# Kernel optimization log

Hardware: AMD Instinct MI355X
Metric: run time of the kernel (lower is better)

The kernel has to match this reference:

```python
import jax, jax.numpy as jnp
import numpy as np

K_DIM = 1024
HEADS = 16


def setup_inputs() -> dict:
    key = jax.random.key(0)
    kx, kw1, kb1, kw2, kb2 = jax.random.split(key, 5)
    b, t, k = 4, 2048, K_DIM
    scale = 1.0 / np.sqrt(k)
    x = jax.random.normal(kx, (b, t, k), dtype=jnp.float32)
    # torch nn.Linear params: weight [out, in], bias [out]
    W_qkv = jax.random.normal(kw1, (3 * k, k), dtype=jnp.float32) * scale
    b_qkv = jax.random.normal(kb1, (3 * k,), dtype=jnp.float32) * scale
    W_out = jax.random.normal(kw2, (k, k), dtype=jnp.float32) * scale
    b_out = jax.random.normal(kb2, (k,), dtype=jnp.float32) * scale
    return {"x": x, "W_qkv": W_qkv, "b_qkv": b_qkv, "W_out": W_out, "b_out": b_out}


def reference(x, W_qkv, b_qkv, W_out, b_out):
    b, t, k = x.shape
    h = HEADS
    s = k // h
    # tokqv linear: [b,t,3k]
    kqv = jnp.einsum('btk,ok->bto', x, W_qkv) + b_qkv
    # view [b,t,h,3s] -> transpose -> [b,h,t,3s], then split q,k,v along last dim
    kqv = kqv.reshape(b, t, h, 3 * s).transpose(0, 2, 1, 3)
    q, kk, v = kqv[..., :s], kqv[..., s:2 * s], kqv[..., 2 * s:]
    scores = jnp.einsum('bhqd,bhkd->bhqk', q, kk) / jnp.sqrt(jnp.float32(s * h))  # note: scale uses full k per source (queries.size(-1)=s, but here head dim s)
    # Faithful: original attention scales by sqrt(queries.size(-1)) = sqrt(s)
    scores = jnp.einsum('bhqd,bhkd->bhqk', q, kk) / jnp.sqrt(jnp.float32(s))
    weights = jax.nn.softmax(scores, axis=-1)
    res = jnp.einsum('bhqk,bhkd->bhqd', weights, v)  # [b,h,t,s]
    res = res.transpose(0, 2, 1, 3).reshape(b, t, k)
    return jnp.einsum('btk,ok->bto', res, W_out) + b_out
```

## Files before the change

### kernel.cpp

```cpp
#include <hip/hip_runtime.h>
#include <hip/hip_bf16.h>

typedef float  f32x4  __attribute__((ext_vector_type(4)));
typedef float  f32x8  __attribute__((ext_vector_type(8)));
typedef float  f32x16 __attribute__((ext_vector_type(16)));
typedef __bf16 bf16x8 __attribute__((ext_vector_type(8)));
typedef unsigned short u16x4 __attribute__((ext_vector_type(4)));
typedef unsigned short u16x8 __attribute__((ext_vector_type(8)));
typedef unsigned int   u32x4 __attribute__((ext_vector_type(4)));

#define QSCALE 0.18033688011112042f

__device__ __forceinline__ unsigned short f2bf(float f) {
  __bf16 h = (__bf16)f;
  return __builtin_bit_cast(unsigned short, h);
}

__device__ __forceinline__ f32x4 mfma16(bf16x8 a, bf16x8 b, f32x4 c) {
  return __builtin_amdgcn_mfma_f32_16x16x32_bf16(a, b, c, 0, 0, 0);
}
__device__ __forceinline__ f32x16 mfma32(bf16x8 a, bf16x8 b, f32x16 c) {
  return __builtin_amdgcn_mfma_f32_32x32x16_bf16(a, b, c, 0, 0, 0);
}
__device__ __forceinline__ f32x16 zero16() {
  f32x16 v;
#pragma unroll
  for (int i = 0; i < 16; ++i) v[i] = 0.f;
  return v;
}

typedef const __attribute__((address_space(1))) void* gptr_t;
typedef __attribute__((address_space(3))) void* lptr_t;
__device__ __forceinline__ void gld16(const void* g, void* l) {
  __builtin_amdgcn_global_load_lds((gptr_t)g, (lptr_t)l, 16, 0, 0);
}


__global__ __launch_bounds__(256) void prep_x(const float* __restrict__ x,
                                              unsigned short* __restrict__ A1) {
  const int mb = blockIdx.x >> 5;
  const int kB = blockIdx.x & 31;
#pragma unroll
  for (int ph = 0; ph < 2; ++ph) {
    int c = threadIdx.x + ph * 256;
    int lg = c >> 7, r = c & 127;
    f32x8 v = *(const f32x8*)(x + (size_t)(mb * 128 + r) * 1024 + kB * 32 + lg * 8);
    u16x8 h;
#pragma unroll
    for (int j = 0; j < 8; ++j) h[j] = f2bf(v[j]);
    *(u16x8*)(A1 + (size_t)(mb * 32 + kB) * 4096 + (size_t)c * 8) = h;
  }
}

__global__ __launch_bounds__(256) void prep_w(const float* __restrict__ w,
                                              unsigned short* __restrict__ o) {
  const int rb = blockIdx.x >> 5;
  const int kB = blockIdx.x & 31;
#pragma unroll
  for (int ph = 0; ph < 2; ++ph) {
    int c = threadIdx.x + ph * 256;
    int lg = c >> 7, r = c & 127;
    f32x8 v = *(const f32x8*)(w + (size_t)(rb * 128 + r) * 1024 + kB * 32 + lg * 8);
    u16x8 h;
#pragma unroll
    for (int j = 0; j < 8; ++j) h[j] = f2bf(v[j]);
    *(u16x8*)(o + (size_t)(rb * 32 + kB) * 4096 + (size_t)c * 8) = h;
  }
}

template <int EPI, int MINW>
__global__ __launch_bounds__(256, MINW) void gemm_bt(
    const __bf16* __restrict__ A, const __bf16* __restrict__ B,
    const float* __restrict__ bias, int N, int nbx, int NT,
    unsigned short* __restrict__ q_out, unsigned short* __restrict__ k_out,
    unsigned short* __restrict__ v_out, float* __restrict__ f_out) {
  __shared__ __align__(16) char smem[3 * 16384];
  const int tid = threadIdx.x;
  const int lane = tid & 63;
  const int wave = tid >> 6;
  const int ln = lane & 15, lg = lane >> 4;
  const int wm = wave >> 1;
  const int wn = wave & 1;
  const int bm = blockIdx.x / nbx;
  const int bn = blockIdx.x % nbx;

  f32x4 acc[4][4];
#pragma unroll
  for (int i = 0; i < 4; ++i)
#pragma unroll
    for (int j = 0; j < 4; ++j) acc[i][j] = (f32x4){0.f, 0.f, 0.f, 0.f};

  const __bf16* Asrc = A + ((size_t)bm * NT) * 4096 + tid * 8;
  const __bf16* Bsrc = B + ((size_t)bn * NT) * 4096 + tid * 8;
  const int aoff = lg * 2048 + (wm * 64 + ln) * 16;
  const int boff = 8192 + lg * 2048 + (wn * 64 + ln) * 16;

#define STAGE(slot_, tf_)                                                      \
  do {                                                                         \
    char* d_ = smem + (slot_) * 16384;                                         \
    const __bf16* a_ = Asrc + (size_t)(tf_) * 4096;                            \
    const __bf16* b_ = Bsrc + (size_t)(tf_) * 4096;                            \
    gld16(a_, d_ + tid * 16);                                                  \
    gld16(a_ + 2048, d_ + 4096 + tid * 16);                                    \
    gld16(b_, d_ + 8192 + tid * 16);                                           \
    gld16(b_ + 2048, d_ + 12288 + tid * 16);                                   \
  } while (0)

#define KBODY(t_, scur_, snxt_)                                                \
  do {                                                                         \
    int tf_ = ((t_) + 2 < NT) ? (t_) + 2 : NT - 1;                             \
    STAGE(snxt_, tf_);                                                         \
    const char* ab_ = smem + (scur_) * 16384;                                  \
    bf16x8 af_[4], bq_[4];                                                     \
    _Pragma("unroll") for (int mi = 0; mi < 4; ++mi)                           \
        af_[mi] = *(const bf16x8*)(ab_ + aoff + mi * 256);                     \
    _Pragma("unroll") for (int ni = 0; ni < 4; ++ni)                           \
        bq_[ni] = *(const bf16x8*)(ab_ + boff + ni * 256);                     \
    __builtin_amdgcn_s_setprio(1);                                             \
    _Pragma("unroll") for (int mi = 0; mi < 4; ++mi)                           \
        _Pragma("unroll") for (int ni = 0; ni < 4; ++ni)                       \
            acc[mi][ni] = mfma16(af_[mi], bq_[ni], acc[mi][ni]);               \
    __builtin_amdgcn_s_setprio(0);                                             \
    asm volatile("s_waitcnt vmcnt(4)\n\ts_barrier" ::: "memory");              \
  } while (0)

  STAGE(0, 0);
  STAGE(1, 1);
  asm volatile("s_waitcnt vmcnt(4)\n\ts_barrier" ::: "memory");

  for (int t = 0; t < NT; t += 3) {
    KBODY(t, 0, 2);
    if (t + 1 < NT) KBODY(t + 1, 1, 0);
    if (t + 2 < NT) KBODY(t + 2, 2, 1);
  }
  asm volatile("s_waitcnt vmcnt(0)" ::: "memory");
#undef KBODY
#undef STAGE

#pragma unroll
  for (int mi = 0; mi < 4; ++mi) {
#pragma unroll
    for (int ni = 0; ni < 4; ++ni) {
      int n = bn * 128 + wn * 64 + ni * 16 + ln;
      float bv = bias[n];
#pragma unroll
      for (int j = 0; j < 4; ++j) {
        int m = bm * 128 + wm * 64 + mi * 16 + lg * 4 + j;
        float val = acc[mi][ni][j] + bv;
        if constexpr (EPI == 0) {
          int h = n / 192;
          int r3 = n - h * 192;
          int b = m >> 11;
          int t = m & 2047;
          size_t base = (size_t)(b * 16 + h) << 17;
          if (r3 < 64) {
            q_out[base + ((size_t)t << 6) + r3] = f2bf(val * QSCALE);
          } else if (r3 < 128) {
            int d = r3 - 64;
            size_t off = base + (size_t)(t >> 6) * 4096 +
                         (size_t)((((t >> 5) & 1) << 2) + (d >> 4)) * 512 +
                         ((d >> 3) & 1) * 256 + (t & 31) * 8 + (d & 7);
            k_out[off] = f2bf(val);
          } else {
            int c = r3 - 128;
            size_t off = base + (size_t)(t >> 6) * 4096 +
                         (size_t)(((c >> 5) << 2) + ((t >> 4) & 3)) * 512 +
                         ((t >> 3) & 1) * 256 + (c & 31) * 8 + (t & 7);
            v_out[off] = f2bf(val);
          }
        } else {
          f_out[(size_t)m * N + n] = val;
        }
      }
    }
  }
}

__global__ __launch_bounds__(512, 4) void attn2(
    const __bf16* __restrict__ Q, const __bf16* __restrict__ Kg,
    const __bf16* __restrict__ Vg, unsigned short* __restrict__ res) {
  __shared__ __align__(16) char smem[3 * 16384];
  const int tid = threadIdx.x;
  const int lane = tid & 63;
  const int wq = tid >> 6;
  const int l31 = lane & 31;
  const int hi = lane >> 5;
  const int bh = blockIdx.x & 63;
  const int q0 = (blockIdx.x >> 6) << 8;
  const size_t bh_elem = (size_t)bh << 17;

  const __bf16* Kbh = Kg + bh_elem;
  const __bf16* Vbh = Vg + bh_elem;

  bf16x8 qf[4];
  {
    const __bf16* qrow = Q + bh_elem + ((size_t)(q0 + wq * 32 + l31) << 6) + hi * 8;
#pragma unroll
    for (int ks = 0; ks < 4; ++ks) qf[ks] = *(const bf16x8*)(qrow + ks * 16);
  }
  const u16x8 one8 = {0x3F80, 0x3F80, 0x3F80, 0x3F80,
                      0x3F80, 0x3F80, 0x3F80, 0x3F80};
  const bf16x8 ones = __builtin_bit_cast(bf16x8, one8);

  const f32x16 fz = zero16();
  f32x16 oacc0 = zero16(), oacc1 = zero16(), lacc = zero16();

#define AST(slot_, t_)                                                         \
  do {                                                                         \
    char* sb_ = smem + (slot_) * 16384;                                        \
    gld16(Kbh + (size_t)(t_) * 4096 + tid * 8, sb_ + tid * 16);                \
    gld16(Vbh + (size_t)(t_) * 4096 + tid * 8, sb_ + 8192 + tid * 16);         \
  } while (0)

  AST(0, 0);
  AST(1, 1);
  asm volatile("s_waitcnt vmcnt(2)\n\ts_barrier" ::: "memory");

  const int t2rev = wq & 1;
  int sc = 0;
  for (int tile = 0; tile < 32; ++tile) {
    int tf = (tile + 2 < 32) ? tile + 2 : 31;
    int sn = sc + 2; if (sn >= 3) sn -= 3;
    AST(sn, tf);

    const char* kbase = smem + sc * 16384;
    const char* vbase = kbase + 8192;
    const int loff = hi * 512 + l31 * 16;

#pragma unroll
    for (int tt = 0; tt < 2; ++tt) {
      const int t2 = tt ^ t2rev;
      f32x16 s;
      __builtin_amdgcn_s_setprio(1);
      {
        bf16x8 kf0 = *(const bf16x8*)(kbase + (t2 * 4) * 1024 + loff);
        s = mfma32(kf0, qf[0], fz);
      }
#pragma unroll
      for (int ks = 1; ks < 4; ++ks) {
        bf16x8 kf = *(const bf16x8*)(kbase + (t2 * 4 + ks) * 1024 + loff);
        s = mfma32(kf, qf[ks], s);
      }
      __builtin_amdgcn_s_setprio(0);
      float p[16];
#pragma unroll
      for (int r = 0; r < 16; ++r) p[r] = __builtin_amdgcn_exp2f(s[r]);
      unsigned int pk[8];
#pragma unroll
      for (int i = 0; i < 8; ++i)
        pk[i] = ((unsigned int)f2bf(p[2 * i + 1]) << 16) | f2bf(p[2 * i]);
      asm volatile("v_permlane32_swap_b32 %0, %1" : "+v"(pk[0]), "+v"(pk[2]));
      asm volatile("v_permlane32_swap_b32 %0, %1" : "+v"(pk[1]), "+v"(pk[3]));
      asm volatile("v_permlane32_swap_b32 %0, %1" : "+v"(pk[4]), "+v"(pk[6]));
      asm volatile("v_permlane32_swap_b32 %0, %1" : "+v"(pk[5]), "+v"(pk[7]));
      __builtin_amdgcn_s_setprio(1);
#pragma unroll
      for (int ks2 = 0; ks2 < 2; ++ks2) {
        u32x4 bw = {pk[ks2 * 4 + 0], pk[ks2 * 4 + 1],
                    pk[ks2 * 4 + 2], pk[ks2 * 4 + 3]};
        bf16x8 pb = __builtin_bit_cast(bf16x8, bw);
        int kb2 = t2 * 2 + ks2;
        bf16x8 v0 = *(const bf16x8*)(vbase + (kb2) * 1024 + loff);
        bf16x8 v1 = *(const bf16x8*)(vbase + (4 + kb2) * 1024 + loff);
        lacc  = mfma32(ones, pb, lacc);
        oacc0 = mfma32(v0, pb, oacc0);
        oacc1 = mfma32(v1, pb, oacc1);
      }
      __builtin_amdgcn_s_setprio(0);
    }
    asm volatile("s_waitcnt vmcnt(2)\n\ts_barrier" ::: "memory");
    sc = (sc + 1 == 3) ? 0 : sc + 1;
  }
  asm volatile("s_waitcnt vmcnt(0)" ::: "memory");
#undef AST

  float rl = __builtin_amdgcn_rcpf(lacc[0]);
  const int b = bh >> 4, h = bh & 15;
  const int rloc = wq * 32 + l31;
  const int mb = b * 16 + (blockIdx.x >> 6) * 2 + (rloc >> 7);
  const int r = rloc & 127;
  unsigned short* c0 = res + (size_t)(mb * 32 + 2 * h) * 4096 + r * 8 + hi * 4;
#pragma unroll
  for (int g = 0; g < 4; ++g) {
    u16x4 st0, st1;
#pragma unroll
    for (int rr = 0; rr < 4; ++rr) {
      st0[rr] = f2bf(oacc0[g * 4 + rr] * rl);
      st1[rr] = f2bf(oacc1[g * 4 + rr] * rl);
    }
    *(u16x4*)(c0 + g * 1024) = st0;
    *(u16x4*)(c0 + 4096 + g * 1024) = st1;
  }
}

extern "C" void kernel_launch(void* const* d_in, const int* in_sizes, int n_in,
                              void* d_out, int out_size, void* d_ws, size_t ws_size,
                              hipStream_t stream) {
  const float* x    = (const float*)d_in[0];
  const float* Wqkv = (const float*)d_in[1];
  const float* bqkv = (const float*)d_in[2];
  const float* Wout = (const float*)d_in[3];
  const float* bout = (const float*)d_in[4];
  float* out = (float*)d_out;
  char* ws = (char*)d_ws;

  unsigned short* A1 = (unsigned short*)(ws);
  unsigned short* B1 = (unsigned short*)(ws + 50331648);
  unsigned short* Qb = (unsigned short*)(ws + 69206016);
  unsigned short* Kb = (unsigned short*)(ws + 85983232);
  unsigned short* Vb = (unsigned short*)(ws + 102760448);
  unsigned short* Rb = (unsigned short*)(ws + 119537664);
  unsigned short* Wo = (unsigned short*)(ws + 136314880);

  prep_x<<<64 * 32, 256, 0, stream>>>(x, A1);
  prep_w<<<24 * 32, 256, 0, stream>>>(Wqkv, B1);
  prep_w<<<8 * 32, 256, 0, stream>>>(Wout, Wo);

  gemm_bt<0, 3><<<64 * 24, 256, 0, stream>>>((const __bf16*)A1, (const __bf16*)B1,
                                             bqkv, 3072, 24, 32,
                                             Qb, Kb, Vb, nullptr);

  attn2<<<512, 512, 0, stream>>>((const __bf16*)Qb, (const __bf16*)Kb,
                                 (const __bf16*)Vb, Rb);

  gemm_bt<1, 2><<<64 * 8, 256, 0, stream>>>((const __bf16*)Rb, (const __bf16*)Wo,
                                            bout, 1024, 8, 32,
                                            nullptr, nullptr, nullptr, out);
}
```

Before: 186.4 us.

## Process two 32-row query blocks per wave in attention kernel

Halves the attention block to 256 threads and has each wave handle 64 query rows (two 32-row Q fragments), so every K and V fragment read from LDS feeds two MFMAs. This is meant to cut LDS read traffic per unit of compute and raise the MFMA-to-load ratio. The cost is more live accumulators and registers per wave, fewer waves per block and lower occupancy (launch bounds 256,2), and twice as many async loads per thread, with the vmcnt waits adjusted to match.

```diff
diff --git a/kernel.cpp b/kernel.cpp
--- a/kernel.cpp
+++ b/kernel.cpp
@@ -176,7 +176,7 @@
   }
 }
 
-__global__ __launch_bounds__(512, 4) void attn2(
+__global__ __launch_bounds__(256, 2) void attn2(
     const __bf16* __restrict__ Q, const __bf16* __restrict__ Kg,
     const __bf16* __restrict__ Vg, unsigned short* __restrict__ res) {
   __shared__ __align__(16) char smem[3 * 16384];
@@ -192,29 +192,37 @@
   const __bf16* Kbh = Kg + bh_elem;
   const __bf16* Vbh = Vg + bh_elem;
 
-  bf16x8 qf[4];
+  bf16x8 qf0[4], qf1[4];
   {
-    const __bf16* qrow = Q + bh_elem + ((size_t)(q0 + wq * 32 + l31) << 6) + hi * 8;
-#pragma unroll
-    for (int ks = 0; ks < 4; ++ks) qf[ks] = *(const bf16x8*)(qrow + ks * 16);
+    const __bf16* qr0 = Q + bh_elem + ((size_t)(q0 + wq * 64 + l31) << 6) + hi * 8;
+    const __bf16* qr1 = qr0 + (32 << 6);
+#pragma unroll
+    for (int ks = 0; ks < 4; ++ks) {
+      qf0[ks] = *(const bf16x8*)(qr0 + ks * 16);
+      qf1[ks] = *(const bf16x8*)(qr1 + ks * 16);
+    }
   }
   const u16x8 one8 = {0x3F80, 0x3F80, 0x3F80, 0x3F80,
                       0x3F80, 0x3F80, 0x3F80, 0x3F80};
   const bf16x8 ones = __builtin_bit_cast(bf16x8, one8);
 
   const f32x16 fz = zero16();
-  f32x16 oacc0 = zero16(), oacc1 = zero16(), lacc = zero16();
+  f32x16 oA0 = zero16(), oA1 = zero16(), lA = zero16();
+  f32x16 oB0 = zero16(), oB1 = zero16(), lB = zero16();
 
 #define AST(slot_, t_)                                                         \
   do {                                                                         \
     char* sb_ = smem + (slot_) * 16384;                                        \
-    gld16(Kbh + (size_t)(t_) * 4096 + tid * 8, sb_ + tid * 16);                \
-    gld16(Vbh + (size_t)(t_) * 4096 + tid * 8, sb_ + 8192 + tid * 16);         \
+    _Pragma("unroll") for (int it_ = 0; it_ < 2; ++it_) {                      \
+      int idx_ = tid + it_ * 256;                                              \
+      gld16(Kbh + (size_t)(t_) * 4096 + idx_ * 8, sb_ + idx_ * 16);            \
+      gld16(Vbh + (size_t)(t_) * 4096 + idx_ * 8, sb_ + 8192 + idx_ * 16);     \
+    }                                                                          \
   } while (0)
 
   AST(0, 0);
   AST(1, 1);
-  asm volatile("s_waitcnt vmcnt(2)\n\ts_barrier" ::: "memory");
+  asm volatile("s_waitcnt vmcnt(4)\n\ts_barrier" ::: "memory");
 
   const int t2rev = wq & 1;
   int sc = 0;
@@ -230,66 +238,91 @@
 #pragma unroll
     for (int tt = 0; tt < 2; ++tt) {
       const int t2 = tt ^ t2rev;
-      f32x16 s;
+      f32x16 s0, s1;
       __builtin_amdgcn_s_setprio(1);
       {
-        bf16x8 kf0 = *(const bf16x8*)(kbase + (t2 * 4) * 1024 + loff);
-        s = mfma32(kf0, qf[0], fz);
+        bf16x8 kf = *(const bf16x8*)(kbase + (t2 * 4) * 1024 + loff);
+        s0 = mfma32(kf, qf0[0], fz);
+        s1 = mfma32(kf, qf1[0], fz);
       }
 #pragma unroll
       for (int ks = 1; ks < 4; ++ks) {
         bf16x8 kf = *(const bf16x8*)(kbase + (t2 * 4 + ks) * 1024 + loff);
-        s = mfma32(kf, qf[ks], s);
+        s0 = mfma32(kf, qf0[ks], s0);
+        s1 = mfma32(kf, qf1[ks], s1);
       }
       __builtin_amdgcn_s_setprio(0);
-      float p[16];
-#pragma unroll
-      for (int r = 0; r < 16; ++r) p[r] = __builtin_amdgcn_exp2f(s[r]);
-      unsigned int pk[8];
-#pragma unroll
-      for (int i = 0; i < 8; ++i)
-        pk[i] = ((unsigned int)f2bf(p[2 * i + 1]) << 16) | f2bf(p[2 * i]);
-      asm volatile("v_permlane32_swap_b32 %0, %1" : "+v"(pk[0]), "+v"(pk[2]));
-      asm volatile("v_permlane32_swap_b32 %0, %1" : "+v"(pk[1]), "+v"(pk[3]));
-      asm volatile("v_permlane32_swap_b32 %0, %1" : "+v"(pk[4]), "+v"(pk[6]));
-      asm volatile("v_permlane32_swap_b32 %0, %1" : "+v"(pk[5]), "+v"(pk[7]));
+      unsigned int pkA[8], pkB[8];
+      {
+        float p[16];
+#pragma unroll
+        for (int r = 0; r < 16; ++r) p[r] = __builtin_amdgcn_exp2f(s0[r]);
+#pragma unroll
+        for (int i = 0; i < 8; ++i)
+          pkA[i] = ((unsigned int)f2bf(p[2 * i + 1]) << 16) | f2bf(p[2 * i]);
+      }
+      {
+        float p[16];
+#pragma unroll
+        for (int r = 0; r < 16; ++r) p[r] = __builtin_amdgcn_exp2f(s1[r]);
+#pragma unroll
+        for (int i = 0; i < 8; ++i)
+          pkB[i] = ((unsigned int)f2bf(p[2 * i + 1]) << 16) | f2bf(p[2 * i]);
+      }
+      asm volatile("v_permlane32_swap_b32 %0, %1" : "+v"(pkA[0]), "+v"(pkA[2]));
+      asm volatile("v_permlane32_swap_b32 %0, %1" : "+v"(pkA[1]), "+v"(pkA[3]));
+      asm volatile("v_permlane32_swap_b32 %0, %1" : "+v"(pkA[4]), "+v"(pkA[6]));
+      asm volatile("v_permlane32_swap_b32 %0, %1" : "+v"(pkA[5]), "+v"(pkA[7]));
+      asm volatile("v_permlane32_swap_b32 %0, %1" : "+v"(pkB[0]), "+v"(pkB[2]));
+      asm volatile("v_permlane32_swap_b32 %0, %1" : "+v"(pkB[1]), "+v"(pkB[3]));
+      asm volatile("v_permlane32_swap_b32 %0, %1" : "+v"(pkB[4]), "+v"(pkB[6]));
+      asm volatile("v_permlane32_swap_b32 %0, %1" : "+v"(pkB[5]), "+v"(pkB[7]));
       __builtin_amdgcn_s_setprio(1);
 #pragma unroll
       for (int ks2 = 0; ks2 < 2; ++ks2) {
-        u32x4 bw = {pk[ks2 * 4 + 0], pk[ks2 * 4 + 1],
-                    pk[ks2 * 4 + 2], pk[ks2 * 4 + 3]};
-        bf16x8 pb = __builtin_bit_cast(bf16x8, bw);
+        u32x4 bwA = {pkA[ks2 * 4 + 0], pkA[ks2 * 4 + 1],
+                     pkA[ks2 * 4 + 2], pkA[ks2 * 4 + 3]};
+        u32x4 bwB = {pkB[ks2 * 4 + 0], pkB[ks2 * 4 + 1],
+                     pkB[ks2 * 4 + 2], pkB[ks2 * 4 + 3]};
+        bf16x8 pbA = __builtin_bit_cast(bf16x8, bwA);
+        bf16x8 pbB = __builtin_bit_cast(bf16x8, bwB);
         int kb2 = t2 * 2 + ks2;
         bf16x8 v0 = *(const bf16x8*)(vbase + (kb2) * 1024 + loff);
         bf16x8 v1 = *(const bf16x8*)(vbase + (4 + kb2) * 1024 + loff);
-        lacc  = mfma32(ones, pb, lacc);
-        oacc0 = mfma32(v0, pb, oacc0);
-        oacc1 = mfma32(v1, pb, oacc1);
+        lA  = mfma32(ones, pbA, lA);
+        oA0 = mfma32(v0, pbA, oA0);
+        oA1 = mfma32(v1, pbA, oA1);
+        lB  = mfma32(ones, pbB, lB);
+        oB0 = mfma32(v0, pbB, oB0);
+        oB1 = mfma32(v1, pbB, oB1);
       }
       __builtin_amdgcn_s_setprio(0);
     }
-    asm volatile("s_waitcnt vmcnt(2)\n\ts_barrier" ::: "memory");
+    asm volatile("s_waitcnt vmcnt(4)\n\ts_barrier" ::: "memory");
     sc = (sc + 1 == 3) ? 0 : sc + 1;
   }
   asm volatile("s_waitcnt vmcnt(0)" ::: "memory");
 #undef AST
 
-  float rl = __builtin_amdgcn_rcpf(lacc[0]);
   const int b = bh >> 4, h = bh & 15;
-  const int rloc = wq * 32 + l31;
-  const int mb = b * 16 + (blockIdx.x >> 6) * 2 + (rloc >> 7);
-  const int r = rloc & 127;
-  unsigned short* c0 = res + (size_t)(mb * 32 + 2 * h) * 4096 + r * 8 + hi * 4;
-#pragma unroll
-  for (int g = 0; g < 4; ++g) {
-    u16x4 st0, st1;
-#pragma unroll
-    for (int rr = 0; rr < 4; ++rr) {
-      st0[rr] = f2bf(oacc0[g * 4 + rr] * rl);
-      st1[rr] = f2bf(oacc1[g * 4 + rr] * rl);
+#pragma unroll
+  for (int g = 0; g < 2; ++g) {
+    float rl = __builtin_amdgcn_rcpf(g ? lB[0] : lA[0]);
+    const int rloc = wq * 64 + g * 32 + l31;
+    const int mb = b * 16 + (blockIdx.x >> 6) * 2 + (rloc >> 7);
+    const int r = rloc & 127;
+    unsigned short* c0 = res + (size_t)(mb * 32 + 2 * h) * 4096 + r * 8 + hi * 4;
+#pragma unroll
+    for (int gg = 0; gg < 4; ++gg) {
+      u16x4 st0, st1;
+#pragma unroll
+      for (int rr = 0; rr < 4; ++rr) {
+        st0[rr] = f2bf((g ? oB0[gg * 4 + rr] : oA0[gg * 4 + rr]) * rl);
+        st1[rr] = f2bf((g ? oB1[gg * 4 + rr] : oA1[gg * 4 + rr]) * rl);
+      }
+      *(u16x4*)(c0 + gg * 1024) = st0;
+      *(u16x4*)(c0 + 4096 + gg * 1024) = st1;
     }
-    *(u16x4*)(c0 + g * 1024) = st0;
-    *(u16x4*)(c0 + 4096 + g * 1024) = st1;
   }
 }
 
@@ -320,7 +353,7 @@
                                              bqkv, 3072, 24, 32,
                                              Qb, Kb, Vb, nullptr);
 
-  attn2<<<512, 512, 0, stream>>>((const __bf16*)Qb, (const __bf16*)Kb,
+  attn2<<<512, 256, 0, stream>>>((const __bf16*)Qb, (const __bf16*)Kb,
                                  (const __bf16*)Vb, Rb);
 
   gemm_bt<1, 2><<<64 * 8, 256, 0, stream>>>((const __bf16*)Rb, (const __bf16*)Wo,
```

New measurement: 188.6 us. Within noise of the previous version (+1.2%).

## Enlarge GEMM tiles to 256x256 with 8 waves and phased double-buffered pipeline

Applied to the files above, without the earlier changes.

Both projection GEMMs now use 256x256 output tiles per 512-thread block (8 waves, each covering 128x64) instead of 128x128 tiles with 4 waves. The K loop becomes a phased schedule: each phase loads A fragments, reuses B fragments across two phases, issues half of the next stage's global-to-LDS copies, and runs 16 MFMAs between barriers, over two 64KB LDS buffers. The aim is more data reuse per byte loaded and better overlap of loads with MFMA work. In exchange it uses 128KB of LDS and more accumulator registers per block, and the out-projection GEMM launches only 128 blocks, which may leave many CUs idle.

```diff
diff --git a/kernel.cpp b/kernel.cpp
--- a/kernel.cpp
+++ b/kernel.cpp
@@ -68,84 +68,104 @@
   }
 }
 
-template <int EPI, int MINW>
-__global__ __launch_bounds__(256, MINW) void gemm_bt(
+template <int EPI>
+__global__ __launch_bounds__(512, 2) void gemm_bt(
     const __bf16* __restrict__ A, const __bf16* __restrict__ B,
-    const float* __restrict__ bias, int N, int nbx, int NT,
+    const float* __restrict__ bias, int N, int nbx,
     unsigned short* __restrict__ q_out, unsigned short* __restrict__ k_out,
     unsigned short* __restrict__ v_out, float* __restrict__ f_out) {
-  __shared__ __align__(16) char smem[3 * 16384];
+  __shared__ __align__(16) char smem[2 * 65536];
   const int tid = threadIdx.x;
   const int lane = tid & 63;
   const int wave = tid >> 6;
   const int ln = lane & 15, lg = lane >> 4;
-  const int wm = wave >> 1;
-  const int wn = wave & 1;
+  const int wm = wave >> 2;
+  const int wn = wave & 3;
   const int bm = blockIdx.x / nbx;
   const int bn = blockIdx.x % nbx;
 
-  f32x4 acc[4][4];
-#pragma unroll
-  for (int i = 0; i < 4; ++i)
+  f32x4 acc[8][4];
+#pragma unroll
+  for (int i = 0; i < 8; ++i)
 #pragma unroll
     for (int j = 0; j < 4; ++j) acc[i][j] = (f32x4){0.f, 0.f, 0.f, 0.f};
 
-  const __bf16* Asrc = A + ((size_t)bm * NT) * 4096 + tid * 8;
-  const __bf16* Bsrc = B + ((size_t)bn * NT) * 4096 + tid * 8;
-  const int aoff = lg * 2048 + (wm * 64 + ln) * 16;
-  const int boff = 8192 + lg * 2048 + (wn * 64 + ln) * 16;
-
-#define STAGE(slot_, tf_)                                                      \
+  const __bf16* Ab0 = A + (size_t)(2 * bm) * 32 * 4096;
+  const __bf16* Bb0 = B + (size_t)(2 * bn) * 32 * 4096;
+  const int aoff = wm * 8192 + lg * 2048 + ln * 16;
+  const int boff = (wn >> 1) * 8192 + lg * 2048 + (wn & 1) * 1024 + ln * 16;
+
+  bf16x8 bq[4];
+
+#define PSTAGE(op_, kb_, sT_, db_)                                             \
   do {                                                                         \
-    char* d_ = smem + (slot_) * 16384;                                         \
-    const __bf16* a_ = Asrc + (size_t)(tf_) * 4096;                            \
-    const __bf16* b_ = Bsrc + (size_t)(tf_) * 4096;                            \
-    gld16(a_, d_ + tid * 16);                                                  \
-    gld16(a_ + 2048, d_ + 4096 + tid * 16);                                    \
-    gld16(b_, d_ + 8192 + tid * 16);                                           \
-    gld16(b_ + 2048, d_ + 12288 + tid * 16);                                   \
+    int kc_ = 2 * (sT_) + (kb_);                                               \
+    const __bf16* s0_ = ((op_) ? Bb0 : Ab0) + (size_t)kc_ * 4096 + tid * 8;    \
+    char* d_ = smem + (db_) * 65536 + (op_) * 32768 + (kb_) * 16384 + tid * 16;\
+    gld16(s0_, d_);                                                            \
+    gld16(s0_ + 32 * 4096, d_ + 8192);                                         \
   } while (0)
 
-#define KBODY(t_, scur_, snxt_)                                                \
+#define PHASE(bp_, kb_, miq_, ldB_, vw_, op_, skb_, sT_, db_)                  \
   do {                                                                         \
-    int tf_ = ((t_) + 2 < NT) ? (t_) + 2 : NT - 1;                             \
-    STAGE(snxt_, tf_);                                                         \
-    const char* ab_ = smem + (scur_) * 16384;                                  \
-    bf16x8 af_[4], bq_[4];                                                     \
-    _Pragma("unroll") for (int mi = 0; mi < 4; ++mi)                           \
-        af_[mi] = *(const bf16x8*)(ab_ + aoff + mi * 256);                     \
-    _Pragma("unroll") for (int ni = 0; ni < 4; ++ni)                           \
-        bq_[ni] = *(const bf16x8*)(ab_ + boff + ni * 256);                     \
+    const char* bc_ = smem + (bp_) * 65536;                                    \
+    bf16x8 af_[4];                                                             \
+    _Pragma("unroll") for (int m_ = 0; m_ < 4; ++m_)                           \
+        af_[m_] = *(const bf16x8*)(bc_ + (kb_) * 16384 + aoff +                \
+                                   ((miq_) * 4 + m_) * 256);                   \
+    if (ldB_) {                                                                \
+      _Pragma("unroll") for (int n_ = 0; n_ < 4; ++n_)                         \
+          bq[n_] = *(const bf16x8*)(bc_ + 32768 + (kb_) * 16384 + boff +       \
+                                    n_ * 256);                                 \
+    }                                                                          \
+    PSTAGE(op_, skb_, sT_, db_);                                               \
+    if (vw_) asm volatile("s_waitcnt vmcnt(8)" ::: "memory");                  \
+    asm volatile("s_barrier" ::: "memory");                                    \
     __builtin_amdgcn_s_setprio(1);                                             \
-    _Pragma("unroll") for (int mi = 0; mi < 4; ++mi)                           \
-        _Pragma("unroll") for (int ni = 0; ni < 4; ++ni)                       \
-            acc[mi][ni] = mfma16(af_[mi], bq_[ni], acc[mi][ni]);               \
+    _Pragma("unroll") for (int m_ = 0; m_ < 4; ++m_)                           \
+        _Pragma("unroll") for (int n_ = 0; n_ < 4; ++n_)                       \
+            acc[(miq_) * 4 + m_][n_] =                                         \
+                mfma16(af_[m_], bq[n_], acc[(miq_) * 4 + m_][n_]);             \
     __builtin_amdgcn_s_setprio(0);                                             \
-    asm volatile("s_waitcnt vmcnt(4)\n\ts_barrier" ::: "memory");              \
+    asm volatile("s_barrier" ::: "memory");                                    \
   } while (0)
 
-  STAGE(0, 0);
-  STAGE(1, 1);
-  asm volatile("s_waitcnt vmcnt(4)\n\ts_barrier" ::: "memory");
-
-  for (int t = 0; t < NT; t += 3) {
-    KBODY(t, 0, 2);
-    if (t + 1 < NT) KBODY(t + 1, 1, 0);
-    if (t + 2 < NT) KBODY(t + 2, 2, 1);
+#define TILE4(P_, s1_, s2_)                                                    \
+  PHASE(P_, 0, 0, 1, 0, 0, 1, s1_, 1 - (P_));                                  \
+  PHASE(P_, 0, 1, 0, 1, 1, 1, s1_, 1 - (P_));                                  \
+  PHASE(P_, 1, 0, 1, 0, 0, 0, s2_, P_);                                        \
+  PHASE(P_, 1, 1, 0, 1, 1, 0, s2_, P_)
+
+  PSTAGE(0, 0, 0, 0);
+  PSTAGE(1, 0, 0, 0);
+  PSTAGE(0, 1, 0, 0);
+  PSTAGE(1, 1, 0, 0);
+  PSTAGE(0, 0, 1, 1);
+  PSTAGE(1, 0, 1, 1);
+  asm volatile("s_waitcnt vmcnt(8)\n\ts_barrier" ::: "memory");
+
+  for (int it = 0; it < 8; ++it) {
+    int T = it * 2;
+    int s1 = T + 1;
+    int s2 = T + 2 < 16 ? T + 2 : 15;
+    int s3 = T + 3 < 16 ? T + 3 : 15;
+    TILE4(0, s1, s2);
+    TILE4(1, s2, s3);
   }
   asm volatile("s_waitcnt vmcnt(0)" ::: "memory");
-#undef KBODY
-#undef STAGE
-
-#pragma unroll
-  for (int mi = 0; mi < 4; ++mi) {
+#undef TILE4
+#undef PHASE
+#undef PSTAGE
+
+#pragma unroll
+  for (int mi = 0; mi < 8; ++mi) {
 #pragma unroll
     for (int ni = 0; ni < 4; ++ni) {
-      int n = bn * 128 + wn * 64 + ni * 16 + ln;
+      int n = bn * 256 + wn * 64 + ni * 16 + ln;
       float bv = bias[n];
 #pragma unroll
       for (int j = 0; j < 4; ++j) {
-        int m = bm * 128 + wm * 64 + mi * 16 + lg * 4 + j;
+        int m = bm * 256 + wm * 128 + mi * 16 + lg * 4 + j;
         float val = acc[mi][ni][j] + bv;
         if constexpr (EPI == 0) {
           int h = n / 192;
@@ -316,14 +336,14 @@
   prep_w<<<24 * 32, 256, 0, stream>>>(Wqkv, B1);
   prep_w<<<8 * 32, 256, 0, stream>>>(Wout, Wo);
 
-  gemm_bt<0, 3><<<64 * 24, 256, 0, stream>>>((const __bf16*)A1, (const __bf16*)B1,
-                                             bqkv, 3072, 24, 32,
-                                             Qb, Kb, Vb, nullptr);
+  gemm_bt<0><<<32 * 12, 512, 0, stream>>>((const __bf16*)A1, (const __bf16*)B1,
+                                          bqkv, 3072, 12,
+                                          Qb, Kb, Vb, nullptr);
 
   attn2<<<512, 512, 0, stream>>>((const __bf16*)Qb, (const __bf16*)Kb,
                                  (const __bf16*)Vb, Rb);
 
-  gemm_bt<1, 2><<<64 * 8, 256, 0, stream>>>((const __bf16*)Rb, (const __bf16*)Wo,
-                                            bout, 1024, 8, 32,
-                                            nullptr, nullptr, nullptr, out);
-}
+  gemm_bt<1><<<32 * 4, 512, 0, stream>>>((const __bf16*)Rb, (const __bf16*)Wo,
+                                         bout, 1024, 4,
+                                         nullptr, nullptr, nullptr, out);
+}
```

Result: slower. 200.7 us (+7.7%).

## Replace triple-buffered single-tile K/V pipeline with double-buffered tile pairs

Applied to the files above, without the earlier changes.

The attention kernel now stages two K/V tiles per shared-memory buffer and alternates between two 32 KB buffers, instead of cycling three 16 KB single-tile slots. This halves the number of loop iterations and the barriers and waitcnt synchronisations per key sequence. The trade-off is that each prefetch is fully awaited (vmcnt(0)) at the end of the iteration that issued it. Total LDS per block also grows from 48 KB to 64 KB, which can lower the number of resident blocks per CU.

```diff
diff --git a/kernel.cpp b/kernel.cpp
--- a/kernel.cpp
+++ b/kernel.cpp
@@ -179,7 +179,7 @@
 __global__ __launch_bounds__(512, 4) void attn2(
     const __bf16* __restrict__ Q, const __bf16* __restrict__ Kg,
     const __bf16* __restrict__ Vg, unsigned short* __restrict__ res) {
-  __shared__ __align__(16) char smem[3 * 16384];
+  __shared__ __align__(16) char smem[2 * 32768];
   const int tid = threadIdx.x;
   const int lane = tid & 63;
   const int wq = tid >> 6;
@@ -205,74 +205,78 @@
   const f32x16 fz = zero16();
   f32x16 oacc0 = zero16(), oacc1 = zero16(), lacc = zero16();
 
-#define AST(slot_, t_)                                                         \
+#define ASTP(s_, p_)                                                           \
   do {                                                                         \
-    char* sb_ = smem + (slot_) * 16384;                                        \
-    gld16(Kbh + (size_t)(t_) * 4096 + tid * 8, sb_ + tid * 16);                \
-    gld16(Vbh + (size_t)(t_) * 4096 + tid * 8, sb_ + 8192 + tid * 16);         \
+    char* sb_ = smem + (s_) * 32768;                                           \
+    const __bf16* k0_ = Kbh + (size_t)(2 * (p_)) * 4096 + tid * 8;             \
+    const __bf16* v0_ = Vbh + (size_t)(2 * (p_)) * 4096 + tid * 8;             \
+    gld16(k0_, sb_ + tid * 16);                                                \
+    gld16(v0_, sb_ + 8192 + tid * 16);                                         \
+    gld16(k0_ + 4096, sb_ + 16384 + tid * 16);                                 \
+    gld16(v0_ + 4096, sb_ + 24576 + tid * 16);                                 \
   } while (0)
 
-  AST(0, 0);
-  AST(1, 1);
-  asm volatile("s_waitcnt vmcnt(2)\n\ts_barrier" ::: "memory");
+  ASTP(0, 0);
+  ASTP(1, 1);
+  asm volatile("s_waitcnt vmcnt(4)\n\ts_barrier" ::: "memory");
 
   const int t2rev = wq & 1;
-  int sc = 0;
-  for (int tile = 0; tile < 32; ++tile) {
-    int tf = (tile + 2 < 32) ? tile + 2 : 31;
-    int sn = sc + 2; if (sn >= 3) sn -= 3;
-    AST(sn, tf);
-
-    const char* kbase = smem + sc * 16384;
-    const char* vbase = kbase + 8192;
+  for (int pr = 0; pr < 16; ++pr) {
+    if (pr >= 1 && pr < 15) ASTP((pr + 1) & 1, pr + 1);
+
+    const char* pbase = smem + (pr & 1) * 32768;
     const int loff = hi * 512 + l31 * 16;
 
 #pragma unroll
-    for (int tt = 0; tt < 2; ++tt) {
-      const int t2 = tt ^ t2rev;
-      f32x16 s;
-      __builtin_amdgcn_s_setprio(1);
-      {
-        bf16x8 kf0 = *(const bf16x8*)(kbase + (t2 * 4) * 1024 + loff);
-        s = mfma32(kf0, qf[0], fz);
+    for (int half = 0; half < 2; ++half) {
+      const char* kbase = pbase + half * 16384;
+      const char* vbase = kbase + 8192;
+
+#pragma unroll
+      for (int tt = 0; tt < 2; ++tt) {
+        const int t2 = tt ^ t2rev;
+        f32x16 s;
+        __builtin_amdgcn_s_setprio(1);
+        {
+          bf16x8 kf0 = *(const bf16x8*)(kbase + (t2 * 4) * 1024 + loff);
+          s = mfma32(kf0, qf[0], fz);
+        }
+#pragma unroll
+        for (int ks = 1; ks < 4; ++ks) {
+          bf16x8 kf = *(const bf16x8*)(kbase + (t2 * 4 + ks) * 1024 + loff);
+          s = mfma32(kf, qf[ks], s);
+        }
+        __builtin_amdgcn_s_setprio(0);
+        float p[16];
+#pragma unroll
+        for (int r = 0; r < 16; ++r) p[r] = __builtin_amdgcn_exp2f(s[r]);
+        unsigned int pk[8];
+#pragma unroll
+        for (int i = 0; i < 8; ++i)
+          pk[i] = ((unsigned int)f2bf(p[2 * i + 1]) << 16) | f2bf(p[2 * i]);
+        asm volatile("v_permlane32_swap_b32 %0, %1" : "+v"(pk[0]), "+v"(pk[2]));
+        asm volatile("v_permlane32_swap_b32 %0, %1" : "+v"(pk[1]), "+v"(pk[3]));
+        asm volatile("v_permlane32_swap_b32 %0, %1" : "+v"(pk[4]), "+v"(pk[6]));
+        asm volatile("v_permlane32_swap_b32 %0, %1" : "+v"(pk[5]), "+v"(pk[7]));
+        __builtin_amdgcn_s_setprio(1);
+#pragma unroll
+        for (int ks2 = 0; ks2 < 2; ++ks2) {
+          u32x4 bw = {pk[ks2 * 4 + 0], pk[ks2 * 4 + 1],
+                      pk[ks2 * 4 + 2], pk[ks2 * 4 + 3]};
+          bf16x8 pb = __builtin_bit_cast(bf16x8, bw);
+          int kb2 = t2 * 2 + ks2;
+          bf16x8 v0 = *(const bf16x8*)(vbase + (kb2) * 1024 + loff);
+          bf16x8 v1 = *(const bf16x8*)(vbase + (4 + kb2) * 1024 + loff);
+          lacc  = mfma32(ones, pb, lacc);
+          oacc0 = mfma32(v0, pb, oacc0);
+          oacc1 = mfma32(v1, pb, oacc1);
+        }
+        __builtin_amdgcn_s_setprio(0);
       }
-#pragma unroll
-      for (int ks = 1; ks < 4; ++ks) {
-        bf16x8 kf = *(const bf16x8*)(kbase + (t2 * 4 + ks) * 1024 + loff);
-        s = mfma32(kf, qf[ks], s);
-      }
-      __builtin_amdgcn_s_setprio(0);
-      float p[16];
-#pragma unroll
-      for (int r = 0; r < 16; ++r) p[r] = __builtin_amdgcn_exp2f(s[r]);
-      unsigned int pk[8];
-#pragma unroll
-      for (int i = 0; i < 8; ++i)
-        pk[i] = ((unsigned int)f2bf(p[2 * i + 1]) << 16) | f2bf(p[2 * i]);
-      asm volatile("v_permlane32_swap_b32 %0, %1" : "+v"(pk[0]), "+v"(pk[2]));
-      asm volatile("v_permlane32_swap_b32 %0, %1" : "+v"(pk[1]), "+v"(pk[3]));
-      asm volatile("v_permlane32_swap_b32 %0, %1" : "+v"(pk[4]), "+v"(pk[6]));
-      asm volatile("v_permlane32_swap_b32 %0, %1" : "+v"(pk[5]), "+v"(pk[7]));
-      __builtin_amdgcn_s_setprio(1);
-#pragma unroll
-      for (int ks2 = 0; ks2 < 2; ++ks2) {
-        u32x4 bw = {pk[ks2 * 4 + 0], pk[ks2 * 4 + 1],
-                    pk[ks2 * 4 + 2], pk[ks2 * 4 + 3]};
-        bf16x8 pb = __builtin_bit_cast(bf16x8, bw);
-        int kb2 = t2 * 2 + ks2;
-        bf16x8 v0 = *(const bf16x8*)(vbase + (kb2) * 1024 + loff);
-        bf16x8 v1 = *(const bf16x8*)(vbase + (4 + kb2) * 1024 + loff);
-        lacc  = mfma32(ones, pb, lacc);
-        oacc0 = mfma32(v0, pb, oacc0);
-        oacc1 = mfma32(v1, pb, oacc1);
-      }
-      __builtin_amdgcn_s_setprio(0);
     }
-    asm volatile("s_waitcnt vmcnt(2)\n\ts_barrier" ::: "memory");
-    sc = (sc + 1 == 3) ? 0 : sc + 1;
-  }
-  asm volatile("s_waitcnt vmcnt(0)" ::: "memory");
-#undef AST
+    asm volatile("s_waitcnt vmcnt(0)\n\ts_barrier" ::: "memory");
+  }
+#undef ASTP
 
   float rl = __builtin_amdgcn_rcpf(lacc[0]);
   const int b = bh >> 4, h = bh & 15;
```

Result: faster. 180.8 us (-3.0%).
